# Kernel optimization log

Measured on AMD Instinct MI355X. Metric: run time of the kernel, lower is better.

The kernel has to match this reference:

```python
import jax, jax.numpy as jnp
import numpy as np

E = 8          # num_experts
TOP_K = 2      # experts per token
D = 1024       # hidden_size
F = 2048       # intermediate_size
B, S = 2, 2048


def setup_inputs() -> dict:
    key = jax.random.key(0)
    k0, k1, k2, k3, k4 = jax.random.split(key, 5)
    return {
        "hidden_states": jax.random.normal(k0, (B, S, D), dtype=jnp.float32),
        "gate_w": jax.random.normal(k1, (D, E), dtype=jnp.float32) * 0.02,
        "w1": jax.random.normal(k2, (E, D, F), dtype=jnp.float32) * 0.02,
        "w2": jax.random.normal(k3, (E, F, D), dtype=jnp.float32) * 0.02,
        "w3": jax.random.normal(k4, (E, D, F), dtype=jnp.float32) * 0.02,
    }


def reference(hidden_states, gate_w, w1, w2, w3):
    b, s, d = hidden_states.shape
    x = hidden_states.reshape(-1, d)                       # [T, D]
    router_logits = x @ gate_w                             # [T, E]
    probs = jax.nn.softmax(router_logits, axis=-1)
    top_w, top_i = jax.lax.top_k(probs, TOP_K)             # [T, K]
    top_w = top_w / jnp.sum(top_w, axis=-1, keepdims=True)

    out = jnp.zeros_like(x)
    for e in range(E):
        # combine weight for expert e per token (0 if not routed here)
        w_e = jnp.sum(jnp.where(top_i == e, top_w, 0.0), axis=-1)   # [T]
        act = jax.nn.silu(x @ w1[e]) * (x @ w3[e])                  # [T, F]
        out = out + (act @ w2[e]) * w_e[:, None]
    return out.reshape(b, s, d)
```

## Files before the change

kernel.cpp:

```cpp
#include <hip/hip_runtime.h>

#define T_TOK 4096
#define D_DIM 1024
#define F_DIM 2048
#define E_NUM 8
#define MAX_TILES 136

typedef __attribute__((ext_vector_type(8))) short bf16x8;
typedef __attribute__((ext_vector_type(4))) float f32x4;

__device__ __forceinline__ unsigned short f2bf(float f) {
  unsigned u = __builtin_bit_cast(unsigned, f);
  unsigned r = 0x7FFFu + ((u >> 16) & 1u);
  return (unsigned short)((u + r) >> 16);
}

__device__ __forceinline__ void gload16(const unsigned short* g, unsigned short* l) {
  __builtin_amdgcn_global_load_lds(
      (const __attribute__((address_space(1))) unsigned int*)g,
      (__attribute__((address_space(3))) unsigned int*)l, 16, 0, 0);
}

__device__ __forceinline__ f32x4 mfma16(bf16x8 a, bf16x8 b, f32x4 c) {
  return __builtin_amdgcn_mfma_f32_16x16x32_bf16(a, b, c, 0, 0, 0);
}

__global__ __launch_bounds__(256) void transpose_all_kernel(
    const float* __restrict__ w1, const float* __restrict__ w3,
    const float* __restrict__ w2,
    unsigned short* __restrict__ W1t, unsigned short* __restrict__ W3t,
    unsigned short* __restrict__ W2t) {
  __shared__ float tile[64][65];
  int z = blockIdx.z;
  int which = z >> 3, e = z & 7;
  const float* src; unsigned short* dst; int M, N;
  if (which == 0)      { src = w1; dst = W1t; M = D_DIM; N = F_DIM; }
  else if (which == 1) { src = w3; dst = W3t; M = D_DIM; N = F_DIM; }
  else                 { src = w2; dst = W2t; M = F_DIM; N = D_DIM; }
  src += (size_t)e * M * N; dst += (size_t)e * M * N;
  int bid = blockIdx.y * gridDim.x + blockIdx.x;
  int nbx = N / 64;
  int i0 = (bid / nbx) * 64, j0 = (bid % nbx) * 64;
  int tid = threadIdx.x;
  int lr = tid >> 4;
  int lc = (tid & 15) * 4;
  #pragma unroll
  for (int p = 0; p < 4; p++) {
    int row = p * 16 + lr;
    float4 v = *(const float4*)&src[(size_t)(i0 + row) * N + j0 + lc];
    tile[row][lc + 0] = v.x; tile[row][lc + 1] = v.y;
    tile[row][lc + 2] = v.z; tile[row][lc + 3] = v.w;
  }
  __syncthreads();
  #pragma unroll
  for (int p = 0; p < 4; p++) {
    int orow = p * 16 + lr;
    unsigned short b0 = f2bf(tile[lc + 0][orow]);
    unsigned short b1 = f2bf(tile[lc + 1][orow]);
    unsigned short b2 = f2bf(tile[lc + 2][orow]);
    unsigned short b3 = f2bf(tile[lc + 3][orow]);
    uint2 o;
    o.x = b0 | ((unsigned)b1 << 16);
    o.y = b2 | ((unsigned)b3 << 16);
    *(uint2*)&dst[(size_t)(j0 + orow) * M + i0 + lc] = o;
  }
}

__global__ __launch_bounds__(256) void logits_kernel(const float* __restrict__ x,
                                                     const float* __restrict__ gw,
                                                     int* __restrict__ route_e,
                                                     float2* __restrict__ route_w,
                                                     unsigned short* __restrict__ Xb) {
  int lane = threadIdx.x & 63;
  int t = blockIdx.x * 4 + (threadIdx.x >> 6);
  float acc[E_NUM];
  #pragma unroll
  for (int e = 0; e < E_NUM; e++) acc[e] = 0.f;
  const float* xr = x + (size_t)t * D_DIM;
  unsigned short* xbr = Xb + (size_t)t * D_DIM;
  #pragma unroll
  for (int j = 0; j < D_DIM / 64; j++) {
    int d = lane + 64 * j;
    float xv = xr[d];
    xbr[d] = f2bf(xv);
    const float4* g = reinterpret_cast<const float4*>(gw + (size_t)d * E_NUM);
    float4 g0 = g[0], g1 = g[1];
    acc[0] += xv * g0.x; acc[1] += xv * g0.y; acc[2] += xv * g0.z; acc[3] += xv * g0.w;
    acc[4] += xv * g1.x; acc[5] += xv * g1.y; acc[6] += xv * g1.z; acc[7] += xv * g1.w;
  }
  #pragma unroll
  for (int e = 0; e < E_NUM; e++) {
    #pragma unroll
    for (int off = 32; off > 0; off >>= 1) acc[e] += __shfl_xor(acc[e], off);
  }
  if (lane == 0) {
    int e1 = 0; float l1 = acc[0];
    #pragma unroll
    for (int e = 1; e < E_NUM; e++) { if (acc[e] > l1) { l1 = acc[e]; e1 = e; } }
    int e2 = -1; float l2 = -1e30f;
    #pragma unroll
    for (int e = 0; e < E_NUM; e++) { if (e != e1 && acc[e] > l2) { l2 = acc[e]; e2 = e; } }
    float wa = 1.f / (1.f + expf(l2 - l1));
    float wb = 1.f / (1.f + expf(l1 - l2));
    route_e[t] = e1 | (e2 << 8);
    route_w[t] = make_float2(wa, wb);
  }
}

__global__ __launch_bounds__(1024) void scatter_kernel(
    const int* __restrict__ route_e, const float2* __restrict__ route_w,
    int* __restrict__ counts, int4* __restrict__ tiles,
    int* __restrict__ list, float* __restrict__ wts) {
  int tid = threadIdx.x;
  int lane = tid & 63, wv = tid >> 6;
  __shared__ int wave_tot[16][E_NUM];
  __shared__ int wave_base[16][E_NUM];
  __shared__ int tot_s[E_NUM];

  int e_loc[8]; float w_loc[8];
  #pragma unroll
  for (int j = 0; j < 4; j++) {
    int t = tid * 4 + j;
    int re = route_e[t];
    float2 rw = route_w[t];
    e_loc[2 * j]     = re & 0xff; w_loc[2 * j]     = rw.x;
    e_loc[2 * j + 1] = re >> 8;   w_loc[2 * j + 1] = rw.y;
  }
  int c[E_NUM], pre[E_NUM];
  #pragma unroll
  for (int e = 0; e < E_NUM; e++) {
    int s = 0;
    #pragma unroll
    for (int j = 0; j < 8; j++) s += (e_loc[j] == e) ? 1 : 0;
    c[e] = s;
  }
  #pragma unroll
  for (int e = 0; e < E_NUM; e++) {
    int v = c[e];
    #pragma unroll
    for (int off = 1; off < 64; off <<= 1) {
      int u = __shfl_up(v, off);
      if (lane >= off) v += u;
    }
    pre[e] = v - c[e];
    if (lane == 63) wave_tot[wv][e] = v;
  }
  __syncthreads();
  if (tid < E_NUM) {
    int s = 0;
    for (int w = 0; w < 16; w++) { wave_base[w][tid] = s; s += wave_tot[w][tid]; }
    tot_s[tid] = s;
    counts[tid] = s;
  }
  __syncthreads();
  #pragma unroll
  for (int j = 0; j < 8; j++) {
    int e = e_loc[j];
    int off = 0;
    #pragma unroll
    for (int jj = 0; jj < 8; jj++)
      if (jj < j) off += (e_loc[jj] == e) ? 1 : 0;
    int basee = 0, pree = 0;
    #pragma unroll
    for (int ee = 0; ee < E_NUM; ee++)
      if (e == ee) { basee = wave_base[wv][ee]; pree = pre[ee]; }
    int pos = basee + pree + off;
    int t = tid * 4 + (j >> 1);
    list[e * T_TOK + pos] = t * 2 + (j & 1);
    wts[e * T_TOK + pos]  = w_loc[j];
  }
  if (tid < MAX_TILES) {
    int4 tt; tt.x = -1; tt.y = 0; tt.z = 0; tt.w = 0;
    int s = 0;
    #pragma unroll
    for (int e = 0; e < E_NUM; e++) {
      int ntl = (tot_s[e] + 63) >> 6;
      if (tid >= s && tid < s + ntl) { tt.x = e; tt.y = (tid - s) * 64; tt.z = tot_s[e]; }
      s += ntl;
    }
    tiles[tid] = tt;
  }
}

__global__ __launch_bounds__(256, 4) void gemm1_kernel(
    const unsigned short* __restrict__ Xb,
    const unsigned short* __restrict__ W1t,
    const unsigned short* __restrict__ W3t,
    const int4* __restrict__ tiles, const int* __restrict__ list,
    unsigned short* __restrict__ H) {
  __shared__ unsigned short As[64 * 64];
  __shared__ unsigned short B1s[64 * 64];
  __shared__ unsigned short B3s[64 * 64];
  __shared__ int rid_s[64];

  int4 td = tiles[blockIdx.y];
  int e = td.x;
  if (e < 0) return;
  int base = td.y, cnt = td.z;
  int nt = blockIdx.x;
  int tid = threadIdx.x;

  if (tid < 64) {
    int r = base + tid; if (r > cnt - 1) r = cnt - 1;
    rid_s[tid] = list[e * T_TOK + r];
  }
  __syncthreads();

  int lane = tid & 63, wid = tid >> 6;
  int sr = lane >> 3;
  int sg = (lane & 7) ^ sr;
  const unsigned short* a_src[2];
  #pragma unroll
  for (int t = 0; t < 2; t++)
    a_src[t] = Xb + (size_t)(rid_s[wid * 16 + t * 8 + sr] >> 1) * D_DIM + sg * 8;
  const unsigned short *b1_src[2], *b3_src[2];
  #pragma unroll
  for (int t = 0; t < 2; t++) {
    size_t row = (size_t)e * F_DIM + nt * 64 + wid * 16 + t * 8 + sr;
    b1_src[t] = W1t + row * D_DIM + sg * 8;
    b3_src[t] = W3t + row * D_DIM + sg * 8;
  }

  int wm = (wid >> 1) * 32, wn = (wid & 1) * 32;
  int frow = lane & 15;
  int fk = lane >> 4;

  unsigned offA[2][2], offB[2][2];
  #pragma unroll
  for (int mf = 0; mf < 2; mf++)
    #pragma unroll
    for (int kc = 0; kc < 2; kc++) {
      int m = wm + mf * 16 + frow, gk = kc * 4 + fk;
      offA[mf][kc] = m * 64 + ((gk ^ (m & 7)) * 8);
    }
  #pragma unroll
  for (int nf = 0; nf < 2; nf++)
    #pragma unroll
    for (int kc = 0; kc < 2; kc++) {
      int n = wn + nf * 16 + frow, gk = kc * 4 + fk;
      offB[nf][kc] = n * 64 + ((gk ^ (n & 7)) * 8);
    }

  f32x4 acc1[2][2], acc3[2][2];
  #pragma unroll
  for (int mf = 0; mf < 2; mf++)
    #pragma unroll
    for (int nf = 0; nf < 2; nf++) {
      f32x4 z = {0.f, 0.f, 0.f, 0.f};
      acc1[mf][nf] = z; acc3[mf][nf] = z;
    }

  #pragma unroll 1
  for (int k0 = 0; k0 < D_DIM; k0 += 64) {
    #pragma unroll
    for (int t = 0; t < 2; t++) {
      gload16(a_src[t] + k0, &As[(wid * 16 + t * 8) * 64]);
      gload16(b1_src[t] + k0, &B1s[(wid * 16 + t * 8) * 64]);
      gload16(b3_src[t] + k0, &B3s[(wid * 16 + t * 8) * 64]);
    }
    __syncthreads();
    #pragma unroll
    for (int kc = 0; kc < 2; kc++) {
      bf16x8 a[2], b1[2], b3[2];
      #pragma unroll
      for (int mf = 0; mf < 2; mf++) a[mf] = *(const bf16x8*)&As[offA[mf][kc]];
      #pragma unroll
      for (int nf = 0; nf < 2; nf++) {
        b1[nf] = *(const bf16x8*)&B1s[offB[nf][kc]];
        b3[nf] = *(const bf16x8*)&B3s[offB[nf][kc]];
      }
      #pragma unroll
      for (int mf = 0; mf < 2; mf++)
        #pragma unroll
        for (int nf = 0; nf < 2; nf++) {
          acc1[mf][nf] = mfma16(a[mf], b1[nf], acc1[mf][nf]);
          acc3[mf][nf] = mfma16(a[mf], b3[nf], acc3[mf][nf]);
        }
    }
    __syncthreads();
  }

  #pragma unroll
  for (int mf = 0; mf < 2; mf++) {
    #pragma unroll
    for (int i = 0; i < 4; i++) {
      int m = wm + mf * 16 + fk * 4 + i;
      if (base + m < cnt) {
        int rid = rid_s[m];
        unsigned short* hrow = H + (size_t)rid * F_DIM + nt * 64 + wn;
        #pragma unroll
        for (int nf = 0; nf < 2; nf++) {
          float z = acc1[mf][nf][i];
          float u = acc3[mf][nf][i];
          hrow[nf * 16 + frow] = f2bf((z / (1.f + expf(-z))) * u);
        }
      }
    }
  }
}

__global__ __launch_bounds__(256, 4) void gemm2_kernel(
    const unsigned short* __restrict__ H,
    const unsigned short* __restrict__ W2t,
    const int4* __restrict__ tiles, const int* __restrict__ list,
    const float* __restrict__ wts,
    float* __restrict__ out) {
  __shared__ unsigned short As[64 * 64];
  __shared__ unsigned short Bs[128 * 64];
  __shared__ int rid_s[64];
  __shared__ float wt_s[64];

  int4 td = tiles[blockIdx.y];
  int e = td.x;
  if (e < 0) return;
  int base = td.y, cnt = td.z;
  int nt = blockIdx.x;
  int tid = threadIdx.x;

  if (tid < 64) {
    int r = base + tid; if (r > cnt - 1) r = cnt - 1;
    rid_s[tid] = list[e * T_TOK + r];
    wt_s[tid] = wts[e * T_TOK + r];
  }
  __syncthreads();

  int lane = tid & 63, wid = tid >> 6;
  int sr = lane >> 3;
  int sg = (lane & 7) ^ sr;
  const unsigned short* a_src[2];
  #pragma unroll
  for (int t = 0; t < 2; t++)
    a_src[t] = H + (size_t)rid_s[wid * 16 + t * 8 + sr] * F_DIM + sg * 8;
  const unsigned short* b_src[4];
  #pragma unroll
  for (int t = 0; t < 4; t++)
    b_src[t] = W2t + ((size_t)e * D_DIM + nt * 128 + wid * 32 + t * 8 + sr) * F_DIM + sg * 8;

  int wm = (wid >> 1) * 32, wn = (wid & 1) * 64;
  int frow = lane & 15;
  int fk = lane >> 4;

  unsigned offA[2][2], offB[4][2];
  #pragma unroll
  for (int mf = 0; mf < 2; mf++)
    #pragma unroll
    for (int kc = 0; kc < 2; kc++) {
      int m = wm + mf * 16 + frow, gk = kc * 4 + fk;
      offA[mf][kc] = m * 64 + ((gk ^ (m & 7)) * 8);
    }
  #pragma unroll
  for (int nf = 0; nf < 4; nf++)
    #pragma unroll
    for (int kc = 0; kc < 2; kc++) {
      int n = wn + nf * 16 + frow, gk = kc * 4 + fk;
      offB[nf][kc] = n * 64 + ((gk ^ (n & 7)) * 8);
    }

  f32x4 acc[2][4];
  #pragma unroll
  for (int mf = 0; mf < 2; mf++)
    #pragma unroll
    for (int nf = 0; nf < 4; nf++) {
      f32x4 z = {0.f, 0.f, 0.f, 0.f};
      acc[mf][nf] = z;
    }

  #pragma unroll 1
  for (int k0 = 0; k0 < F_DIM; k0 += 64) {
    #pragma unroll
    for (int t = 0; t < 2; t++)
      gload16(a_src[t] + k0, &As[(wid * 16 + t * 8) * 64]);
    #pragma unroll
    for (int t = 0; t < 4; t++)
      gload16(b_src[t] + k0, &Bs[(wid * 32 + t * 8) * 64]);
    __syncthreads();
    #pragma unroll
    for (int kc = 0; kc < 2; kc++) {
      bf16x8 a[2], b[4];
      #pragma unroll
      for (int mf = 0; mf < 2; mf++) a[mf] = *(const bf16x8*)&As[offA[mf][kc]];
      #pragma unroll
      for (int nf = 0; nf < 4; nf++) b[nf] = *(const bf16x8*)&Bs[offB[nf][kc]];
      #pragma unroll
      for (int mf = 0; mf < 2; mf++)
        #pragma unroll
        for (int nf = 0; nf < 4; nf++)
          acc[mf][nf] = mfma16(a[mf], b[nf], acc[mf][nf]);
    }
    __syncthreads();
  }

  #pragma unroll
  for (int mf = 0; mf < 2; mf++) {
    #pragma unroll
    for (int i = 0; i < 4; i++) {
      int m = wm + mf * 16 + fk * 4 + i;
      if (base + m < cnt) {
        int tok = rid_s[m] >> 1;
        float w = wt_s[m];
        float* orow = out + (size_t)tok * D_DIM + nt * 128 + wn;
        #pragma unroll
        for (int nf = 0; nf < 4; nf++)
          atomicAdd(&orow[nf * 16 + frow], acc[mf][nf][i] * w);
      }
    }
  }
}

extern "C" void kernel_launch(void* const* d_in, const int* in_sizes, int n_in,
                              void* d_out, int out_size, void* d_ws, size_t ws_size,
                              hipStream_t stream) {
  const float* x  = (const float*)d_in[0];
  const float* gw = (const float*)d_in[1];
  const float* w1 = (const float*)d_in[2];
  const float* w2 = (const float*)d_in[3];
  const float* w3 = (const float*)d_in[4];
  float* out = (float*)d_out;

  char* ws = (char*)d_ws;
  const size_t LISTB = (size_t)E_NUM * T_TOK * 4;
  size_t o_counts  = 0;
  size_t o_tiles   = 256;
  size_t o_route_e = 4096;
  size_t o_route_w = o_route_e + (size_t)T_TOK * 4;
  size_t o_list    = o_route_w + (size_t)T_TOK * 8;
  size_t o_wts     = o_list + LISTB;
  size_t o_Xb      = o_wts + LISTB;
  size_t o_W1t     = o_Xb + (size_t)T_TOK * D_DIM * 2;
  size_t wt_sz     = (size_t)E_NUM * F_DIM * D_DIM * 2;
  size_t o_W3t     = o_W1t + wt_sz;
  size_t o_W2t     = o_W3t + wt_sz;
  size_t o_H       = o_W2t + wt_sz;

  int* counts   = (int*)(ws + o_counts);
  int4* tiles   = (int4*)(ws + o_tiles);
  int* route_e  = (int*)(ws + o_route_e);
  float2* route_w = (float2*)(ws + o_route_w);
  int* list     = (int*)(ws + o_list);
  float* wts    = (float*)(ws + o_wts);
  unsigned short* Xb  = (unsigned short*)(ws + o_Xb);
  unsigned short* W1t = (unsigned short*)(ws + o_W1t);
  unsigned short* W3t = (unsigned short*)(ws + o_W3t);
  unsigned short* W2t = (unsigned short*)(ws + o_W2t);
  unsigned short* H   = (unsigned short*)(ws + o_H);

  hipMemsetAsync(out, 0, (size_t)out_size * 4, stream);

  transpose_all_kernel<<<dim3(32, 16, 24), 256, 0, stream>>>(
      w1, w3, w2, W1t, W3t, W2t);

  logits_kernel<<<dim3(T_TOK / 4), 256, 0, stream>>>(x, gw, route_e, route_w, Xb);
  scatter_kernel<<<dim3(1), 1024, 0, stream>>>(route_e, route_w, counts, tiles, list, wts);

  gemm1_kernel<<<dim3(F_DIM / 64, MAX_TILES), 256, 0, stream>>>(
      Xb, W1t, W3t, tiles, list, H);
  gemm2_kernel<<<dim3(D_DIM / 128, MAX_TILES), 256, 0, stream>>>(
      H, W2t, tiles, list, wts, out);
}
```

Measured before the change: 241.1 us.

## Merge weight transpose and router into one launch; gemm1 loops over two N-tiles

The weight transpose/convert and the router-logits kernels become a single prep kernel, with extra z-slices handling the logits. This removes one launch and lets the small routing work overlap the big transpose. gemm1 now has each block process two consecutive 64-wide F tiles in sequence, halving its grid and reusing the block's row-id setup and A-fragment offsets. The A tile is still reloaded from global memory for each pass, and the smaller grid may lower occupancy and parallelism in gemm1.

```diff
diff --git a/kernel.cpp b/kernel.cpp
--- a/kernel.cpp
+++ b/kernel.cpp
@@ -8,14 +8,15 @@
 
 typedef __attribute__((ext_vector_type(8))) short bf16x8;
 typedef __attribute__((ext_vector_type(4))) float f32x4;
-
-__device__ __forceinline__ unsigned short f2bf(float f) {
+typedef unsigned short us;
+
+__device__ __forceinline__ us f2bf(float f) {
   unsigned u = __builtin_bit_cast(unsigned, f);
   unsigned r = 0x7FFFu + ((u >> 16) & 1u);
-  return (unsigned short)((u + r) >> 16);
-}
-
-__device__ __forceinline__ void gload16(const unsigned short* g, unsigned short* l) {
+  return (us)((u + r) >> 16);
+}
+
+__device__ __forceinline__ void gload16(const us* g, us* l) {
   __builtin_amdgcn_global_load_lds(
       (const __attribute__((address_space(1))) unsigned int*)g,
       (__attribute__((address_space(3))) unsigned int*)l, 16, 0, 0);
@@ -25,85 +26,84 @@
   return __builtin_amdgcn_mfma_f32_16x16x32_bf16(a, b, c, 0, 0, 0);
 }
 
-__global__ __launch_bounds__(256) void transpose_all_kernel(
+__global__ __launch_bounds__(256) void prep_kernel(
     const float* __restrict__ w1, const float* __restrict__ w3,
     const float* __restrict__ w2,
-    unsigned short* __restrict__ W1t, unsigned short* __restrict__ W3t,
-    unsigned short* __restrict__ W2t) {
-  __shared__ float tile[64][65];
+    us* __restrict__ W1t, us* __restrict__ W3t, us* __restrict__ W2t,
+    const float* __restrict__ x, const float* __restrict__ gw,
+    int* __restrict__ route_e, float2* __restrict__ route_w,
+    us* __restrict__ Xb) {
   int z = blockIdx.z;
-  int which = z >> 3, e = z & 7;
-  const float* src; unsigned short* dst; int M, N;
-  if (which == 0)      { src = w1; dst = W1t; M = D_DIM; N = F_DIM; }
-  else if (which == 1) { src = w3; dst = W3t; M = D_DIM; N = F_DIM; }
-  else                 { src = w2; dst = W2t; M = F_DIM; N = D_DIM; }
-  src += (size_t)e * M * N; dst += (size_t)e * M * N;
-  int bid = blockIdx.y * gridDim.x + blockIdx.x;
-  int nbx = N / 64;
-  int i0 = (bid / nbx) * 64, j0 = (bid % nbx) * 64;
   int tid = threadIdx.x;
-  int lr = tid >> 4;
-  int lc = (tid & 15) * 4;
-  #pragma unroll
-  for (int p = 0; p < 4; p++) {
-    int row = p * 16 + lr;
-    float4 v = *(const float4*)&src[(size_t)(i0 + row) * N + j0 + lc];
-    tile[row][lc + 0] = v.x; tile[row][lc + 1] = v.y;
-    tile[row][lc + 2] = v.z; tile[row][lc + 3] = v.w;
-  }
-  __syncthreads();
-  #pragma unroll
-  for (int p = 0; p < 4; p++) {
-    int orow = p * 16 + lr;
-    unsigned short b0 = f2bf(tile[lc + 0][orow]);
-    unsigned short b1 = f2bf(tile[lc + 1][orow]);
-    unsigned short b2 = f2bf(tile[lc + 2][orow]);
-    unsigned short b3 = f2bf(tile[lc + 3][orow]);
-    uint2 o;
-    o.x = b0 | ((unsigned)b1 << 16);
-    o.y = b2 | ((unsigned)b3 << 16);
-    *(uint2*)&dst[(size_t)(j0 + orow) * M + i0 + lc] = o;
-  }
-}
-
-__global__ __launch_bounds__(256) void logits_kernel(const float* __restrict__ x,
-                                                     const float* __restrict__ gw,
-                                                     int* __restrict__ route_e,
-                                                     float2* __restrict__ route_w,
-                                                     unsigned short* __restrict__ Xb) {
-  int lane = threadIdx.x & 63;
-  int t = blockIdx.x * 4 + (threadIdx.x >> 6);
-  float acc[E_NUM];
-  #pragma unroll
-  for (int e = 0; e < E_NUM; e++) acc[e] = 0.f;
-  const float* xr = x + (size_t)t * D_DIM;
-  unsigned short* xbr = Xb + (size_t)t * D_DIM;
-  #pragma unroll
-  for (int j = 0; j < D_DIM / 64; j++) {
-    int d = lane + 64 * j;
-    float xv = xr[d];
-    xbr[d] = f2bf(xv);
-    const float4* g = reinterpret_cast<const float4*>(gw + (size_t)d * E_NUM);
-    float4 g0 = g[0], g1 = g[1];
-    acc[0] += xv * g0.x; acc[1] += xv * g0.y; acc[2] += xv * g0.z; acc[3] += xv * g0.w;
-    acc[4] += xv * g1.x; acc[5] += xv * g1.y; acc[6] += xv * g1.z; acc[7] += xv * g1.w;
-  }
-  #pragma unroll
-  for (int e = 0; e < E_NUM; e++) {
-    #pragma unroll
-    for (int off = 32; off > 0; off >>= 1) acc[e] += __shfl_xor(acc[e], off);
-  }
-  if (lane == 0) {
-    int e1 = 0; float l1 = acc[0];
-    #pragma unroll
-    for (int e = 1; e < E_NUM; e++) { if (acc[e] > l1) { l1 = acc[e]; e1 = e; } }
-    int e2 = -1; float l2 = -1e30f;
-    #pragma unroll
-    for (int e = 0; e < E_NUM; e++) { if (e != e1 && acc[e] > l2) { l2 = acc[e]; e2 = e; } }
-    float wa = 1.f / (1.f + expf(l2 - l1));
-    float wb = 1.f / (1.f + expf(l1 - l2));
-    route_e[t] = e1 | (e2 << 8);
-    route_w[t] = make_float2(wa, wb);
+
+  if (z < 24) {
+    __shared__ float tile[64][65];
+    int which = z >> 3, e = z & 7;
+    const float* src; us* dst; int M, N;
+    if (which == 0)      { src = w1; dst = W1t; M = D_DIM; N = F_DIM; }
+    else if (which == 1) { src = w3; dst = W3t; M = D_DIM; N = F_DIM; }
+    else                 { src = w2; dst = W2t; M = F_DIM; N = D_DIM; }
+    src += (size_t)e * M * N; dst += (size_t)e * M * N;
+    int bid = blockIdx.y * gridDim.x + blockIdx.x;
+    int nbx = N / 64;
+    int i0 = (bid / nbx) * 64, j0 = (bid % nbx) * 64;
+    int lr = tid >> 4, lc = (tid & 15) * 4;
+    #pragma unroll
+    for (int p = 0; p < 4; p++) {
+      int row = p * 16 + lr;
+      float4 v = *(const float4*)&src[(size_t)(i0 + row) * N + j0 + lc];
+      tile[row][lc + 0] = v.x; tile[row][lc + 1] = v.y;
+      tile[row][lc + 2] = v.z; tile[row][lc + 3] = v.w;
+    }
+    __syncthreads();
+    #pragma unroll
+    for (int p = 0; p < 4; p++) {
+      int orow = p * 16 + lr;
+      us b0 = f2bf(tile[lc + 0][orow]);
+      us b1 = f2bf(tile[lc + 1][orow]);
+      us b2 = f2bf(tile[lc + 2][orow]);
+      us b3 = f2bf(tile[lc + 3][orow]);
+      uint2 o;
+      o.x = b0 | ((unsigned)b1 << 16);
+      o.y = b2 | ((unsigned)b3 << 16);
+      *(uint2*)&dst[(size_t)(j0 + orow) * M + i0 + lc] = o;
+    }
+  } else {
+    int bid = (z - 24) * 512 + blockIdx.y * gridDim.x + blockIdx.x;
+    int lane = tid & 63;
+    int t = bid * 4 + (tid >> 6);
+    float acc[E_NUM];
+    #pragma unroll
+    for (int e = 0; e < E_NUM; e++) acc[e] = 0.f;
+    const float* xr = x + (size_t)t * D_DIM;
+    us* xbr = Xb + (size_t)t * D_DIM;
+    #pragma unroll
+    for (int j = 0; j < D_DIM / 64; j++) {
+      int d = lane + 64 * j;
+      float xv = xr[d];
+      xbr[d] = f2bf(xv);
+      const float4* g = reinterpret_cast<const float4*>(gw + (size_t)d * E_NUM);
+      float4 g0 = g[0], g1 = g[1];
+      acc[0] += xv * g0.x; acc[1] += xv * g0.y; acc[2] += xv * g0.z; acc[3] += xv * g0.w;
+      acc[4] += xv * g1.x; acc[5] += xv * g1.y; acc[6] += xv * g1.z; acc[7] += xv * g1.w;
+    }
+    #pragma unroll
+    for (int e = 0; e < E_NUM; e++) {
+      #pragma unroll
+      for (int off = 32; off > 0; off >>= 1) acc[e] += __shfl_xor(acc[e], off);
+    }
+    if (lane == 0) {
+      int e1 = 0; float l1 = acc[0];
+      #pragma unroll
+      for (int e = 1; e < E_NUM; e++) { if (acc[e] > l1) { l1 = acc[e]; e1 = e; } }
+      int e2 = -1; float l2 = -1e30f;
+      #pragma unroll
+      for (int e = 0; e < E_NUM; e++) { if (e != e1 && acc[e] > l2) { l2 = acc[e]; e2 = e; } }
+      float wa = 1.f / (1.f + expf(l2 - l1));
+      float wb = 1.f / (1.f + expf(l1 - l2));
+      route_e[t] = e1 | (e2 << 8);
+      route_w[t] = make_float2(wa, wb);
+    }
   }
 }
 
@@ -183,15 +183,136 @@
 }
 
 __global__ __launch_bounds__(256, 4) void gemm1_kernel(
-    const unsigned short* __restrict__ Xb,
-    const unsigned short* __restrict__ W1t,
-    const unsigned short* __restrict__ W3t,
+    const us* __restrict__ Xb,
+    const us* __restrict__ W1t,
+    const us* __restrict__ W3t,
     const int4* __restrict__ tiles, const int* __restrict__ list,
-    unsigned short* __restrict__ H) {
-  __shared__ unsigned short As[64 * 64];
-  __shared__ unsigned short B1s[64 * 64];
-  __shared__ unsigned short B3s[64 * 64];
+    us* __restrict__ H) {
+  __shared__ us As[64 * 64];
+  __shared__ us B1s[64 * 64];
+  __shared__ us B3s[64 * 64];
   __shared__ int rid_s[64];
+
+  int4 td = tiles[blockIdx.y];
+  int e = td.x;
+  if (e < 0) return;
+  int base = td.y, cnt = td.z;
+  int tid = threadIdx.x;
+
+  if (tid < 64) {
+    int r = base + tid; if (r > cnt - 1) r = cnt - 1;
+    rid_s[tid] = list[e * T_TOK + r];
+  }
+  __syncthreads();
+
+  int lane = tid & 63, wid = tid >> 6;
+  int sr = lane >> 3;
+  int sg = (lane & 7) ^ sr;
+  const us* a_src[2];
+  #pragma unroll
+  for (int t = 0; t < 2; t++)
+    a_src[t] = Xb + (size_t)(rid_s[wid * 16 + t * 8 + sr] >> 1) * D_DIM + sg * 8;
+
+  int wm = (wid >> 1) * 32, wn = (wid & 1) * 32;
+  int frow = lane & 15;
+  int fk = lane >> 4;
+
+  unsigned offA[2][2], offB[2][2];
+  #pragma unroll
+  for (int mf = 0; mf < 2; mf++)
+    #pragma unroll
+    for (int kc = 0; kc < 2; kc++) {
+      int m = wm + mf * 16 + frow, gk = kc * 4 + fk;
+      offA[mf][kc] = m * 64 + ((gk ^ (m & 7)) * 8);
+    }
+  #pragma unroll
+  for (int nf = 0; nf < 2; nf++)
+    #pragma unroll
+    for (int kc = 0; kc < 2; kc++) {
+      int n = wn + nf * 16 + frow, gk = kc * 4 + fk;
+      offB[nf][kc] = n * 64 + ((gk ^ (n & 7)) * 8);
+    }
+
+  #pragma unroll 1
+  for (int rep = 0; rep < 2; rep++) {
+    int nt = blockIdx.x * 2 + rep;
+    const us *b1_src[2], *b3_src[2];
+    #pragma unroll
+    for (int t = 0; t < 2; t++) {
+      size_t row = (size_t)e * F_DIM + nt * 64 + wid * 16 + t * 8 + sr;
+      b1_src[t] = W1t + row * D_DIM + sg * 8;
+      b3_src[t] = W3t + row * D_DIM + sg * 8;
+    }
+
+    f32x4 acc1[2][2], acc3[2][2];
+    #pragma unroll
+    for (int mf = 0; mf < 2; mf++)
+      #pragma unroll
+      for (int nf = 0; nf < 2; nf++) {
+        f32x4 z = {0.f, 0.f, 0.f, 0.f};
+        acc1[mf][nf] = z; acc3[mf][nf] = z;
+      }
+
+    #pragma unroll 1
+    for (int k0 = 0; k0 < D_DIM; k0 += 64) {
+      #pragma unroll
+      for (int t = 0; t < 2; t++) {
+        gload16(a_src[t] + k0, &As[(wid * 16 + t * 8) * 64]);
+        gload16(b1_src[t] + k0, &B1s[(wid * 16 + t * 8) * 64]);
+        gload16(b3_src[t] + k0, &B3s[(wid * 16 + t * 8) * 64]);
+      }
+      __syncthreads();
+      #pragma unroll
+      for (int kc = 0; kc < 2; kc++) {
+        bf16x8 a[2], b1[2], b3[2];
+        #pragma unroll
+        for (int mf = 0; mf < 2; mf++) a[mf] = *(const bf16x8*)&As[offA[mf][kc]];
+        #pragma unroll
+        for (int nf = 0; nf < 2; nf++) {
+          b1[nf] = *(const bf16x8*)&B1s[offB[nf][kc]];
+          b3[nf] = *(const bf16x8*)&B3s[offB[nf][kc]];
+        }
+        #pragma unroll
+        for (int mf = 0; mf < 2; mf++)
+          #pragma unroll
+          for (int nf = 0; nf < 2; nf++) {
+            acc1[mf][nf] = mfma16(a[mf], b1[nf], acc1[mf][nf]);
+            acc3[mf][nf] = mfma16(a[mf], b3[nf], acc3[mf][nf]);
+          }
+      }
+      __syncthreads();
+    }
+
+    #pragma unroll
+    for (int mf = 0; mf < 2; mf++) {
+      #pragma unroll
+      for (int i = 0; i < 4; i++) {
+        int m = wm + mf * 16 + fk * 4 + i;
+        if (base + m < cnt) {
+          int rid = rid_s[m];
+          us* hrow = H + (size_t)rid * F_DIM + nt * 64 + wn;
+          #pragma unroll
+          for (int nf = 0; nf < 2; nf++) {
+            float z = acc1[mf][nf][i];
+            float u = acc3[mf][nf][i];
+            hrow[nf * 16 + frow] = f2bf((z / (1.f + expf(-z))) * u);
+          }
+        }
+      }
+    }
+  }
+}
+
+__global__ __launch_bounds__(256, 4) void gemm2_kernel(
+    const us* __restrict__ H,
+    const us* __restrict__ W2t,
+    const int4* __restrict__ tiles, const int* __restrict__ list,
+    const float* __restrict__ wts,
+    float* __restrict__ out) {
+  __shared__ us As[64 * 64];
+  __shared__ us Bs[128 * 64];
+  __shared__ int rid_s[64];
+  __shared__ float wt_s[64];
 
   int4 td = tiles[blockIdx.y];
   int e = td.x;
@@ -203,135 +324,18 @@
   if (tid < 64) {
     int r = base + tid; if (r > cnt - 1) r = cnt - 1;
     rid_s[tid] = list[e * T_TOK + r];
+    wt_s[tid] = wts[e * T_TOK + r];
   }
   __syncthreads();
 
   int lane = tid & 63, wid = tid >> 6;
   int sr = lane >> 3;
   int sg = (lane & 7) ^ sr;
-  const unsigned short* a_src[2];
-  #pragma unroll
-  for (int t = 0; t < 2; t++)
-    a_src[t] = Xb + (size_t)(rid_s[wid * 16 + t * 8 + sr] >> 1) * D_DIM + sg * 8;
-  const unsigned short *b1_src[2], *b3_src[2];
-  #pragma unroll
-  for (int t = 0; t < 2; t++) {
-    size_t row = (size_t)e * F_DIM + nt * 64 + wid * 16 + t * 8 + sr;
-    b1_src[t] = W1t + row * D_DIM + sg * 8;
-    b3_src[t] = W3t + row * D_DIM + sg * 8;
-  }
-
-  int wm = (wid >> 1) * 32, wn = (wid & 1) * 32;
-  int frow = lane & 15;
-  int fk = lane >> 4;
-
-  unsigned offA[2][2], offB[2][2];
-  #pragma unroll
-  for (int mf = 0; mf < 2; mf++)
-    #pragma unroll
-    for (int kc = 0; kc < 2; kc++) {
-      int m = wm + mf * 16 + frow, gk = kc * 4 + fk;
-      offA[mf][kc] = m * 64 + ((gk ^ (m & 7)) * 8);
-    }
-  #pragma unroll
-  for (int nf = 0; nf < 2; nf++)
-    #pragma unroll
-    for (int kc = 0; kc < 2; kc++) {
-      int n = wn + nf * 16 + frow, gk = kc * 4 + fk;
-      offB[nf][kc] = n * 64 + ((gk ^ (n & 7)) * 8);
-    }
-
-  f32x4 acc1[2][2], acc3[2][2];
-  #pragma unroll
-  for (int mf = 0; mf < 2; mf++)
-    #pragma unroll
-    for (int nf = 0; nf < 2; nf++) {
-      f32x4 z = {0.f, 0.f, 0.f, 0.f};
-      acc1[mf][nf] = z; acc3[mf][nf] = z;
-    }
-
-  #pragma unroll 1
-  for (int k0 = 0; k0 < D_DIM; k0 += 64) {
-    #pragma unroll
-    for (int t = 0; t < 2; t++) {
-      gload16(a_src[t] + k0, &As[(wid * 16 + t * 8) * 64]);
-      gload16(b1_src[t] + k0, &B1s[(wid * 16 + t * 8) * 64]);
-      gload16(b3_src[t] + k0, &B3s[(wid * 16 + t * 8) * 64]);
-    }
-    __syncthreads();
-    #pragma unroll
-    for (int kc = 0; kc < 2; kc++) {
-      bf16x8 a[2], b1[2], b3[2];
-      #pragma unroll
-      for (int mf = 0; mf < 2; mf++) a[mf] = *(const bf16x8*)&As[offA[mf][kc]];
-      #pragma unroll
-      for (int nf = 0; nf < 2; nf++) {
-        b1[nf] = *(const bf16x8*)&B1s[offB[nf][kc]];
-        b3[nf] = *(const bf16x8*)&B3s[offB[nf][kc]];
-      }
-      #pragma unroll
-      for (int mf = 0; mf < 2; mf++)
-        #pragma unroll
-        for (int nf = 0; nf < 2; nf++) {
-          acc1[mf][nf] = mfma16(a[mf], b1[nf], acc1[mf][nf]);
-          acc3[mf][nf] = mfma16(a[mf], b3[nf], acc3[mf][nf]);
-        }
-    }
-    __syncthreads();
-  }
-
-  #pragma unroll
-  for (int mf = 0; mf < 2; mf++) {
-    #pragma unroll
-    for (int i = 0; i < 4; i++) {
-      int m = wm + mf * 16 + fk * 4 + i;
-      if (base + m < cnt) {
-        int rid = rid_s[m];
-        unsigned short* hrow = H + (size_t)rid * F_DIM + nt * 64 + wn;
-        #pragma unroll
-        for (int nf = 0; nf < 2; nf++) {
-          float z = acc1[mf][nf][i];
-          float u = acc3[mf][nf][i];
-          hrow[nf * 16 + frow] = f2bf((z / (1.f + expf(-z))) * u);
-        }
-      }
-    }
-  }
-}
-
-__global__ __launch_bounds__(256, 4) void gemm2_kernel(
-    const unsigned short* __restrict__ H,
-    const unsigned short* __restrict__ W2t,
-    const int4* __restrict__ tiles, const int* __restrict__ list,
-    const float* __restrict__ wts,
-    float* __restrict__ out) {
-  __shared__ unsigned short As[64 * 64];
-  __shared__ unsigned short Bs[128 * 64];
-  __shared__ int rid_s[64];
-  __shared__ float wt_s[64];
-
-  int4 td = tiles[blockIdx.y];
-  int e = td.x;
-  if (e < 0) return;
-  int base = td.y, cnt = td.z;
-  int nt = blockIdx.x;
-  int tid = threadIdx.x;
-
-  if (tid < 64) {
-    int r = base + tid; if (r > cnt - 1) r = cnt - 1;
-    rid_s[tid] = list[e * T_TOK + r];
-    wt_s[tid] = wts[e * T_TOK + r];
-  }
-  __syncthreads();
-
-  int lane = tid & 63, wid = tid >> 6;
-  int sr = lane >> 3;
-  int sg = (lane & 7) ^ sr;
-  const unsigned short* a_src[2];
+  const us* a_src[2];
   #pragma unroll
   for (int t = 0; t < 2; t++)
     a_src[t] = H + (size_t)rid_s[wid * 16 + t * 8 + sr] * F_DIM + sg * 8;
-  const unsigned short* b_src[4];
+  const us* b_src[4];
   #pragma unroll
   for (int t = 0; t < 4; t++)
     b_src[t] = W2t + ((size_t)e * D_DIM + nt * 128 + wid * 32 + t * 8 + sr) * F_DIM + sg * 8;
@@ -432,27 +436,27 @@
   size_t o_W2t     = o_W3t + wt_sz;
   size_t o_H       = o_W2t + wt_sz;
 
-  int* counts   = (int*)(ws + o_counts);
-  int4* tiles   = (int4*)(ws + o_tiles);
-  int* route_e  = (int*)(ws + o_route_e);
+  int* counts    = (int*)(ws + o_counts);
+  int4* tiles    = (int4*)(ws + o_tiles);
+  int* route_e   = (int*)(ws + o_route_e);
   float2* route_w = (float2*)(ws + o_route_w);
-  int* list     = (int*)(ws + o_list);
-  float* wts    = (float*)(ws + o_wts);
-  unsigned short* Xb  = (unsigned short*)(ws + o_Xb);
-  unsigned short* W1t = (unsigned short*)(ws + o_W1t);
-  unsigned short* W3t = (unsigned short*)(ws + o_W3t);
-  unsigned short* W2t = (unsigned short*)(ws + o_W2t);
-  unsigned short* H   = (unsigned short*)(ws + o_H);
+  int* list      = (int*)(ws + o_list);
+  float* wts     = (float*)(ws + o_wts);
+  us* Xb  = (us*)(ws + o_Xb);
+  us* W1t = (us*)(ws + o_W1t);
+  us* W3t = (us*)(ws + o_W3t);
+  us* W2t = (us*)(ws + o_W2t);
+  us* H   = (us*)(ws + o_H);
 
   hipMemsetAsync(out, 0, (size_t)out_size * 4, stream);
 
-  transpose_all_kernel<<<dim3(32, 16, 24), 256, 0, stream>>>(
-      w1, w3, w2, W1t, W3t, W2t);
-
-  logits_kernel<<<dim3(T_TOK / 4), 256, 0, stream>>>(x, gw, route_e, route_w, Xb);
-  scatter_kernel<<<dim3(1), 1024, 0, stream>>>(route_e, route_w, counts, tiles, list, wts);
-
-  gemm1_kernel<<<dim3(F_DIM / 64, MAX_TILES), 256, 0, stream>>>(
+  prep_kernel<<<dim3(32, 16, 26), 256, 0, stream>>>(
+      w1, w3, w2, W1t, W3t, W2t, x, gw, route_e, route_w, Xb);
+
+  scatter_kernel<<<dim3(1), 1024, 0, stream>>>(route_e, route_w, counts,
+                                               tiles, list, wts);
+
+  gemm1_kernel<<<dim3(F_DIM / 128, MAX_TILES), 256, 0, stream>>>(
       Xb, W1t, W3t, tiles, list, H);
   gemm2_kernel<<<dim3(D_DIM / 128, MAX_TILES), 256, 0, stream>>>(
       H, W2t, tiles, list, wts, out);
```

After: 245.0 us. Within noise of the previous version (+1.6%).
